# Kernel optimization log

Hardware: AMD Instinct MI355X
Metric: run time of the kernel (lower is better)

Reference implementation:

```python
import jax, jax.numpy as jnp
import numpy as np

NUM_NODES = 120000   # entity count
D = 128              # graph_emb_size
T = 10               # time_steps / train_year
B = 64               # batch of input_ids
R = 4                # num_rel
N = 64               # max neighbors per relation (padded)
C = 64               # TCN channel width (output_size)
I = 64               # influence_emb_size
K = 2                # kernel size
L = 8                # TCN levels (num_channels = [64]*8)


def _causal_conv(x, w, b, d):
    # x: [M, Cin, T], w: [Cout, Cin, k] -> causal dilated conv -> [M, Cout, T]
    pad = (w.shape[-1] - 1) * d
    y = jax.lax.conv_general_dilated(x, w, window_strides=(1,), padding=[(pad, 0)],
                                     rhs_dilation=(d,), dimension_numbers=('NCH', 'OIH', 'NCH'))
    return y + b[None, :, None]


def _tcn_last(x, w1_0, b1_0, w2_0, b2_0, down_w, down_b, w1, b1, w2, b2):
    # Bai-style TemporalConvNet; x: [M, D, T] -> last-step state [M, C]
    y = jax.nn.relu(_causal_conv(x, w1_0, b1_0, 1))
    y = jax.nn.relu(_causal_conv(y, w2_0, b2_0, 1))
    h = jax.nn.relu(y + _causal_conv(x, down_w, down_b, 1))  # 1x1 downsample residual (Cin != C)
    for i in range(1, L):
        d = 2 ** i
        y = jax.nn.relu(_causal_conv(h, w1[i - 1], b1[i - 1], d))
        y = jax.nn.relu(_causal_conv(y, w2[i - 1], b2[i - 1], d))
        h = jax.nn.relu(y + h)
    return h[..., -1]


def setup_inputs() -> dict:
    key = jax.random.key(0)
    ks = jax.random.split(key, 16)
    embeddings = jax.random.normal(ks[0], (T, NUM_NODES, D), jnp.float32)
    # entity -> per-year row index; negative = entity absent that year (zero-padded)
    alignment = jax.random.randint(ks[1], (NUM_NODES, T), -NUM_NODES // 5, NUM_NODES).astype(jnp.int32)
    neighbor_idx = jax.random.randint(ks[2], (B, R, N), 0, NUM_NODES).astype(jnp.int32)
    neighbor_mask = jax.random.randint(ks[3], (B, R, N), 0, 2).astype(bool)
    g = lambda k, sh, s: jax.random.normal(k, sh, jnp.float32) * s
    return {
        'embeddings': embeddings,
        'w1_0': g(ks[4], (R, C, D, K), (2.0 / (D * K)) ** 0.5),
        'b1_0': jnp.zeros((R, C), jnp.float32),
        'w2_0': g(ks[5], (R, C, C, K), (2.0 / (C * K)) ** 0.5),
        'b2_0': jnp.zeros((R, C), jnp.float32),
        'down_w': g(ks[6], (R, C, D, 1), (2.0 / D) ** 0.5),
        'down_b': jnp.zeros((R, C), jnp.float32),
        'w1': g(ks[7], (R, L - 1, C, C, K), (2.0 / (C * K)) ** 0.5),
        'b1': jnp.zeros((R, L - 1, C), jnp.float32),
        'w2': g(ks[8], (R, L - 1, C, C, K), (2.0 / (C * K)) ** 0.5),
        'b2': jnp.zeros((R, L - 1, C), jnp.float32),
        'rel_w': g(ks[9], (R, C, I), (2.0 / (C + I)) ** 0.5),
        'alignment': alignment,
        'neighbor_idx': neighbor_idx,
        'neighbor_mask': neighbor_mask,
    }


def reference(embeddings, w1_0, b1_0, w2_0, b2_0, down_w, down_b, w1, b1, w2, b2,
              rel_w, alignment, neighbor_idx, neighbor_mask):
    seq = alignment[neighbor_idx]                                   # [B,R,N,T]
    valid = (seq >= 0) & neighbor_mask[..., None]                   # per-year + existence mask
    idx = jnp.clip(seq, 0)
    # per-year gather: embeddings[t][idx[...,t]] -> [B,R,N,D,T]
    gath = jax.vmap(lambda e, i: e[i], in_axes=(0, -1), out_axes=-1)(embeddings, idx)
    x = gath * valid[:, :, :, None, :].astype(gath.dtype)           # zero-pad absent years
    x = jnp.transpose(x, (1, 0, 2, 3, 4)).reshape(R, B * N, D, T)   # relation-major, neighbors as batch
    last = jax.vmap(_tcn_last)(x, w1_0, b1_0, w2_0, b2_0, down_w, down_b, w1, b1, w2, b2)  # [R,B*N,C]
    infl = jnp.einsum('rmc,rci->rmi', last, rel_w).reshape(R, B, N, I)
    m = jnp.transpose(neighbor_mask, (1, 0, 2)).astype(infl.dtype)  # [R,B,N] drop padded neighbors
    return jnp.einsum('rbni,rbn->bi', infl, m)                      # sum over neighbors and relations
```

## Files before the change

kernel.cpp:

```cpp
#include <hip/hip_runtime.h>
#include <hip/hip_bf16.h>
#include <stdint.h>

constexpr int NUM_NODES = 120000;
constexpr int Tn = 10;
constexpr int Bb = 64, Rr = 4, Nn = 64, Cc = 64, Ii = 64;
constexpr int RSTR  = 147456;
constexpr int OFF0  = 0;
constexpr int OFF1  = 16384;
constexpr int OFF2  = 24576;
constexpr int OFFL0 = 32768;

constexpr int OFF_X  = 0;
constexpr int OFF_H0 = 0;
constexpr int OFF_H1 = 10240;
constexpr int OFF_H2 = 16384;
constexpr int OFF_H3 = 20480;
constexpr int OFF_Y  = 40960;
constexpr int ZOFF   = 61440;
constexpr int SMEMB  = 61696;

typedef __attribute__((ext_vector_type(8))) short bf16x8;
typedef __attribute__((ext_vector_type(4))) float f32x4;
typedef __attribute__((ext_vector_type(4))) short s16x4;

__device__ __forceinline__ short f2bf(float f) {
  __hip_bfloat16 h = __float2bfloat16(f);
  return *reinterpret_cast<short*>(&h);
}
__device__ __forceinline__ float bf2f(short s) {
  union { unsigned int u; float f; } x;
  x.u = ((unsigned int)(unsigned short)s) << 16;
  return x.f;
}

extern "C" __global__ void prep_kernel(const float* __restrict__ w1_0,
                                       const float* __restrict__ w2_0,
                                       const float* __restrict__ down_w,
                                       const float* __restrict__ w1s,
                                       const float* __restrict__ w2s,
                                       short* __restrict__ Wf) {
  int i0 = blockIdx.x * blockDim.x + threadIdx.x;
  int stride = gridDim.x * blockDim.x;
  for (int e = i0; e < Rr * RSTR; e += stride) {
    int r = e / RSTR, q = e - r * RSTR;
    float v;
    if (q < 16384) {
      int j = q & 7, lane = (q >> 3) & 63, ks = (q >> 9) & 3, ct = (q >> 11) & 3, tap = (q >> 13) & 1;
      int cout = ct * 16 + (lane & 15), cin = ks * 32 + (lane >> 4) * 8 + j;
      v = w1_0[((r * 64 + cout) * 128 + cin) * 2 + tap];
    } else if (q < 24576) {
      int q2 = q - 16384;
      int j = q2 & 7, lane = (q2 >> 3) & 63, ks = (q2 >> 9) & 3, ct = (q2 >> 11) & 3;
      int cout = ct * 16 + (lane & 15), cin = ks * 32 + (lane >> 4) * 8 + j;
      v = down_w[(r * 64 + cout) * 128 + cin];
    } else if (q < 32768) {
      int q2 = q - 24576;
      int j = q2 & 7, lane = (q2 >> 3) & 63, ks = (q2 >> 9) & 1, ct = (q2 >> 10) & 3, tap = (q2 >> 12) & 1;
      int cout = ct * 16 + (lane & 15), cin = ks * 32 + (lane >> 4) * 8 + j;
      v = w2_0[((r * 64 + cout) * 64 + cin) * 2 + tap];
    } else {
      int q2 = q - 32768;
      int lc = q2 >> 13;
      int l = lc >> 1, jw = lc & 1;
      int q3 = q2 & 8191;
      int j = q3 & 7, lane = (q3 >> 3) & 63, ks = (q3 >> 9) & 1, ct = (q3 >> 10) & 3, tap = (q3 >> 12) & 1;
      int cout = ct * 16 + (lane & 15), cin = ks * 32 + (lane >> 4) * 8 + j;
      const float* src = jw ? w2s : w1s;
      v = src[(((r * 7 + l) * 64 + cout) * 64 + cin) * 2 + tap];
    }
    Wf[e] = f2bf(v);
  }
}

template <int KSN, int NMT, int NTAP, int ROWB>
__device__ __forceinline__ void conv_sp(const char* __restrict__ sm, int srcOff,
                                        const short* __restrict__ wf1,
                                        const short* __restrict__ wf0,
                                        const float* __restrict__ bias,
                                        const int (&T1)[NMT], const int (&T0)[NMT],
                                        int lane, int ct, f32x4 (&acc)[NMT]) {
  const int c16 = (lane >> 4) * 16;
  const int sw = (lane & 7) << 4;
  const int cm = lane & 15;
  float bv[4];
#pragma unroll
  for (int g = 0; g < 4; ++g) bv[g] = bias[ct * 16 + (lane >> 4) * 4 + g];
#pragma unroll
  for (int mt = 0; mt < NMT; ++mt) acc[mt] = (f32x4){bv[0], bv[1], bv[2], bv[3]};
  bf16x8 af1[KSN], af0[KSN];
#pragma unroll
  for (int ks = 0; ks < KSN; ++ks)
    af1[ks] = *(const bf16x8*)(wf1 + ((ct * KSN + ks) * 64 + lane) * 8);
  if (NTAP == 2) {
#pragma unroll
    for (int ks = 0; ks < KSN; ++ks)
      af0[ks] = *(const bf16x8*)(wf0 + ((ct * KSN + ks) * 64 + lane) * 8);
  }
#pragma unroll
  for (int mt = 0; mt < NMT; ++mt) {
    int s1 = T1[mt];
    const char* p1 = sm + ((s1 < 0) ? ZOFF : srcOff + (s1 * 16 + cm) * ROWB);
#pragma unroll
    for (int ks = 0; ks < KSN; ++ks) {
      bf16x8 b = *(const bf16x8*)(p1 + ((ks * 64 + c16) ^ sw));
      acc[mt] = __builtin_amdgcn_mfma_f32_16x16x32_bf16(af1[ks], b, acc[mt], 0, 0, 0);
    }
    if (NTAP == 2) {
      int s0 = T0[mt];
      const char* p0 = sm + ((s0 < 0) ? ZOFF : srcOff + (s0 * 16 + cm) * ROWB);
#pragma unroll
      for (int ks = 0; ks < KSN; ++ks) {
        bf16x8 b = *(const bf16x8*)(p0 + ((ks * 64 + c16) ^ sw));
        acc[mt] = __builtin_amdgcn_mfma_f32_16x16x32_bf16(af0[ks], b, acc[mt], 0, 0, 0);
      }
    }
  }
}

template <int NMT>
__device__ __forceinline__ void store_sp(char* __restrict__ sm, int dstOff, int s0,
                                         int lane, int ct, const f32x4 (&v)[NMT]) {
  const int co = ct * 32 + (lane >> 4) * 8;
  const int sw = (lane & 7) << 4;
#pragma unroll
  for (int mt = 0; mt < NMT; ++mt) {
    int oc = (s0 + mt) * 16 + (lane & 15);
    s16x4 p;
#pragma unroll
    for (int g = 0; g < 4; ++g) p[g] = f2bf(v[mt][g]);
    *(s16x4*)(sm + dstOff + oc * 128 + (co ^ sw)) = p;
  }
}

#define RELU_ALL(A, N)                                        \
  _Pragma("unroll") for (int _t = 0; _t < N; ++_t)            \
      _Pragma("unroll") for (int _g = 0; _g < 4; ++_g)        \
          A[_t][_g] = fmaxf(A[_t][_g], 0.f);

template <int NMT>
__device__ __forceinline__ void resid_sp(const char* __restrict__ sm, int prevOff,
                                         const int (&R)[NMT], int lane, int ct,
                                         f32x4 (&a)[NMT]) {
  const int co = ct * 32 + (lane >> 4) * 8;
  const int sw = (lane & 7) << 4;
  const int cm = lane & 15;
#pragma unroll
  for (int mt = 0; mt < NMT; ++mt) {
    const char* p = sm + prevOff + (R[mt] * 16 + cm) * 128;
    s16x4 q = *(const s16x4*)(p + (co ^ sw));
#pragma unroll
    for (int g = 0; g < 4; ++g)
      a[mt][g] = fmaxf(fmaxf(a[mt][g], 0.f) + bf2f(q[g]), 0.f);
  }
}

extern "C" __global__ void __launch_bounds__(512, 4)
tcn_mfma(const float* __restrict__ emb, const int* __restrict__ align_,
         const int* __restrict__ nidx, const int* __restrict__ nmask,
         const float* __restrict__ b1_0, const float* __restrict__ b2_0,
         const float* __restrict__ down_b, const float* __restrict__ b1s,
         const float* __restrict__ b2s, const short* __restrict__ Wf,
         float* __restrict__ P) {
  __shared__ char sm[SMEMB];
  __shared__ int rowid[160];
  __shared__ float mkv[16];
  __shared__ int mapg[16];
  __shared__ int totv;

  const int tid = threadIdx.x;
  const int lane = tid & 63, wave = tid >> 6;
  const int ct = wave & 3, half = wave >> 2;
  const int blk = blockIdx.x;
  const int r = blk >> 8;
  const int b = (blk >> 2) & 63, chunk = blk & 3;

  if (tid < 64) {
    int n = tid;
    int msk = nmask[(b * Rr + r) * Nn + n];
    unsigned long long bal = __ballot(msk != 0);
    if (tid < 16) mapg[tid] = -1;
    if (tid == 0) totv = (int)__popcll(bal);
    int rank = (int)__popcll(bal & ((1ull << n) - 1ull));
    if (msk != 0 && rank >= chunk * 16 && rank < chunk * 16 + 16)
      mapg[rank - chunk * 16] = n;
  }
  if (tid >= 448 && tid < 480) *(uint64_t*)(sm + ZOFF + (tid - 448) * 8) = 0;
  __syncthreads();
  if (chunk * 16 >= totv) {
    if (tid < 64) P[((r * Bb + b) * 4 + chunk) * 64 + tid] = 0.f;
    return;
  }

  if (tid < 160) {
    int t = tid >> 4, seq = tid & 15;
    int n2 = mapg[seq];
    int s = -1;
    if (n2 >= 0) {
      int ent = nidx[(b * Rr + r) * Nn + n2];
      s = align_[ent * Tn + t];
    }
    rowid[tid] = (n2 >= 0 && s >= 0) ? s : -1;
    if (t == 0) mkv[seq] = (n2 >= 0) ? 1.0f : 0.0f;
  }
  __syncthreads();

#pragma unroll
  for (int it = 0; it < 10; ++it) {
    int idx = tid + it * 512;
    int col = idx >> 5, d4 = idx & 31;
    int row = rowid[col];
    int t = col >> 4;
    s16x4 p = {0, 0, 0, 0};
    if (row >= 0) {
      const float4 v = *(const float4*)(emb + ((size_t)t * NUM_NODES + row) * 128 + d4 * 4);
      p[0] = f2bf(v.x); p[1] = f2bf(v.y); p[2] = f2bf(v.z); p[3] = f2bf(v.w);
    }
    *(s16x4*)(sm + OFF_X + col * 256 + ((d4 * 8) ^ ((col & 7) << 4))) = p;
  }
  __syncthreads();

  const short* wr = Wf + r * RSTR;

  {
    static constexpr int T1a[5] = {0, 1, 2, 3, 4}, T0a[5] = {-1, 0, 1, 2, 3};
    static constexpr int T1b[5] = {5, 6, 7, 8, 9}, T0b[5] = {4, 5, 6, 7, 8};
    f32x4 a[5];
    conv_sp<4, 5, 2, 256>(sm, OFF_X, wr + OFF0 + 8192, wr + OFF0, b1_0 + r * 64,
                          half ? T1b : T1a, half ? T0b : T0a, lane, ct, a);
    RELU_ALL(a, 5)
    store_sp<5>(sm, OFF_Y, half ? 5 : 0, lane, ct, a);
  }
  f32x4 accD[3];
  {
    static constexpr int TDa[3] = {1, 3, 5}, TDb[3] = {5, 7, 9};
    conv_sp<4, 3, 1, 256>(sm, OFF_X, wr + OFF1, wr + OFF1, down_b + r * 64,
                          half ? TDb : TDa, half ? TDb : TDa, lane, ct, accD);
  }
  __syncthreads();
  {
    static constexpr int T1a[3] = {1, 3, 5}, T0a[3] = {0, 2, 4};
    static constexpr int T1b[3] = {5, 7, 9}, T0b[3] = {4, 6, 8};
    f32x4 a[3];
    conv_sp<2, 3, 2, 128>(sm, OFF_Y, wr + OFF2 + 4096, wr + OFF2, b2_0 + r * 64,
                          half ? T1b : T1a, half ? T0b : T0a, lane, ct, a);
#pragma unroll
    for (int mt = 0; mt < 3; ++mt)
#pragma unroll
      for (int g = 0; g < 4; ++g)
        a[mt][g] = fmaxf(fmaxf(a[mt][g], 0.f) + accD[mt][g], 0.f);
    store_sp<3>(sm, OFF_H0, half ? 2 : 0, lane, ct, a);
  }
  __syncthreads();
  {
    static constexpr int T1a[3] = {0, 1, 2}, T0a[3] = {-1, 0, 1};
    static constexpr int T1b[3] = {2, 3, 4}, T0b[3] = {1, 2, 3};
    const short* wl = wr + OFFL0;
    f32x4 a[3];
    conv_sp<2, 3, 2, 128>(sm, OFF_H0, wl + 4096, wl, b1s + (r * 7 + 0) * 64,
                          half ? T1b : T1a, half ? T0b : T0a, lane, ct, a);
    RELU_ALL(a, 3)
    store_sp<3>(sm, OFF_Y, half ? 2 : 0, lane, ct, a);
  }
  __syncthreads();
  {
    static constexpr int T1a[2] = {0, 2}, T0a[2] = {-1, 1}, Ra[2] = {0, 2};
    static constexpr int T1b[2] = {2, 4}, T0b[2] = {1, 3}, Rb[2] = {2, 4};
    const short* wl = wr + OFFL0 + 8192;
    f32x4 a[2];
    conv_sp<2, 2, 2, 128>(sm, OFF_Y, wl + 4096, wl, b2s + (r * 7 + 0) * 64,
                          half ? T1b : T1a, half ? T0b : T0a, lane, ct, a);
    resid_sp<2>(sm, OFF_H0, half ? Rb : Ra, lane, ct, a);
    store_sp<2>(sm, OFF_H1, half ? 1 : 0, lane, ct, a);
  }
  __syncthreads();
  {
    static constexpr int T1a[2] = {0, 1}, T0a[2] = {-1, 0};
    static constexpr int T1b[2] = {1, 2}, T0b[2] = {0, 1};
    const short* wl = wr + OFFL0 + 16384;
    f32x4 a[2];
    conv_sp<2, 2, 2, 128>(sm, OFF_H1, wl + 4096, wl, b1s + (r * 7 + 1) * 64,
                          half ? T1b : T1a, half ? T0b : T0a, lane, ct, a);
    RELU_ALL(a, 2)
    store_sp<2>(sm, OFF_Y, half ? 1 : 0, lane, ct, a);
  }
  __syncthreads();
  {
    static constexpr int T1a[1] = {0}, T0a[1] = {-1}, Ra[1] = {0};
    static constexpr int T1b[1] = {2}, T0b[1] = {1}, Rb[1] = {2};
    const short* wl = wr + OFFL0 + 16384 + 8192;
    f32x4 a[1];
    conv_sp<2, 1, 2, 128>(sm, OFF_Y, wl + 4096, wl, b2s + (r * 7 + 1) * 64,
                          half ? T1b : T1a, half ? T0b : T0a, lane, ct, a);
    resid_sp<1>(sm, OFF_H1, half ? Rb : Ra, lane, ct, a);
    store_sp<1>(sm, OFF_H2, half ? 1 : 0, lane, ct, a);
  }
  __syncthreads();
  {
    static constexpr int T1a[1] = {0}, T0a[1] = {-1};
    static constexpr int T1b[1] = {1}, T0b[1] = {0};
    const short* wl = wr + OFFL0 + 32768;
    f32x4 a[1];
    conv_sp<2, 1, 2, 128>(sm, OFF_H2, wl + 4096, wl, b1s + (r * 7 + 2) * 64,
                          half ? T1b : T1a, half ? T0b : T0a, lane, ct, a);
    RELU_ALL(a, 1)
    store_sp<1>(sm, OFF_Y, half ? 1 : 0, lane, ct, a);
  }
  __syncthreads();
  {
    static constexpr int T1c[1] = {1}, T0c[1] = {0}, Rc[1] = {1};
    const short* wl = wr + OFFL0 + 32768 + 8192;
    f32x4 a[1];
    conv_sp<2, 1, 2, 128>(sm, OFF_Y, wl + 4096, wl, b2s + (r * 7 + 2) * 64,
                          T1c, T0c, lane, ct, a);
    resid_sp<1>(sm, OFF_H2, Rc, lane, ct, a);
    store_sp<1>(sm, OFF_H3, 0, lane, ct, a);
  }
  __syncthreads();

  if (wave != 0) return;

  f32x4 hfin[4];
  static constexpr int TA[1] = {0};
#pragma unroll 1
  for (int li = 0; li < 4; ++li) {
    const short* base = wr + OFFL0 + (3 + li) * 16384;
    const int prevOff = OFF_H3 + li * 2048;
#pragma unroll
    for (int c2 = 0; c2 < 4; ++c2) {
      f32x4 a[1];
      conv_sp<2, 1, 1, 128>(sm, prevOff, base + 4096, base + 4096,
                            b1s + (r * 7 + 3 + li) * 64, TA, TA, lane, c2, a);
      RELU_ALL(a, 1)
      store_sp<1>(sm, OFF_Y, 0, lane, c2, a);
    }
    __builtin_amdgcn_s_waitcnt(0);
    __builtin_amdgcn_sched_barrier(0);
#pragma unroll
    for (int c2 = 0; c2 < 4; ++c2) {
      f32x4 a[1];
      conv_sp<2, 1, 1, 128>(sm, OFF_Y, base + 8192 + 4096, base + 8192 + 4096,
                            b2s + (r * 7 + 3 + li) * 64, TA, TA, lane, c2, a);
      resid_sp<1>(sm, prevOff, TA, lane, c2, a);
      if (li < 3) store_sp<1>(sm, prevOff + 2048, 0, lane, c2, a);
      hfin[c2] = a[0];
    }
    __builtin_amdgcn_s_waitcnt(0);
    __builtin_amdgcn_sched_barrier(0);
  }

  float mk = mkv[lane & 15];
#pragma unroll
  for (int c2 = 0; c2 < 4; ++c2) {
    float s0 = hfin[c2][0] * mk, s1 = hfin[c2][1] * mk;
    float s2 = hfin[c2][2] * mk, s3 = hfin[c2][3] * mk;
#pragma unroll
    for (int m2 = 1; m2 <= 8; m2 <<= 1) {
      s0 += __shfl_xor(s0, m2);
      s1 += __shfl_xor(s1, m2);
      s2 += __shfl_xor(s2, m2);
      s3 += __shfl_xor(s3, m2);
    }
    if ((lane & 15) == 0) {
      int base = ((r * Bb + b) * 4 + chunk) * 64 + c2 * 16 + (lane >> 4) * 4;
      P[base + 0] = s0;
      P[base + 1] = s1;
      P[base + 2] = s2;
      P[base + 3] = s3;
    }
  }
}

extern "C" __global__ void reduce_kernel(const float* __restrict__ P,
                                         const float* __restrict__ rel_w,
                                         float* __restrict__ out) {
  __shared__ float Sl[Rr * Cc];
  int b = blockIdx.x, i = threadIdx.x;
  for (int idx = i; idx < Rr * Cc; idx += 64) {
    int rr = idx >> 6, cc = idx & 63;
    float s = 0.f;
    for (int p = 0; p < 4; ++p) s += P[((rr * Bb + b) * 4 + p) * 64 + cc];
    Sl[idx] = s;
  }
  __syncthreads();
  float acc = 0.f;
  for (int r = 0; r < Rr; ++r)
#pragma unroll
    for (int cc = 0; cc < 64; ++cc)
      acc += Sl[r * Cc + cc] * rel_w[(r * Cc + cc) * Ii + i];
  out[b * Ii + i] = acc;
}

extern "C" void kernel_launch(void* const* d_in, const int* in_sizes, int n_in,
                              void* d_out, int out_size, void* d_ws, size_t ws_size,
                              hipStream_t stream) {
  const float* emb    = (const float*)d_in[0];
  const float* w1_0   = (const float*)d_in[1];
  const float* b1_0   = (const float*)d_in[2];
  const float* w2_0   = (const float*)d_in[3];
  const float* b2_0   = (const float*)d_in[4];
  const float* down_w = (const float*)d_in[5];
  const float* down_b = (const float*)d_in[6];
  const float* w1s    = (const float*)d_in[7];
  const float* b1s    = (const float*)d_in[8];
  const float* w2s    = (const float*)d_in[9];
  const float* b2s    = (const float*)d_in[10];
  const float* rel_w  = (const float*)d_in[11];
  const int* align_   = (const int*)d_in[12];
  const int* nidx     = (const int*)d_in[13];
  const int* nmask    = (const int*)d_in[14];

  float* P  = (float*)d_ws;
  short* Wf = (short*)((char*)d_ws + 524288);

  prep_kernel<<<768, 256, 0, stream>>>(w1_0, w2_0, down_w, w1s, w2s, Wf);
  tcn_mfma<<<1024, 512, 0, stream>>>(emb, align_, nidx, nmask, b1_0, b2_0, down_b,
                                     b1s, b2s, Wf, P);
  reduce_kernel<<<Bb, Cc, 0, stream>>>(P, rel_w, (float*)d_out);
}
```

Baseline: 63.00 us.

## Process 32 neighbors per block with 4 waves sharing weight fragments across two tiles

```diff
diff --git a/kernel.cpp b/kernel.cpp
--- a/kernel.cpp
+++ b/kernel.cpp
@@ -4,7 +4,7 @@
 
 constexpr int NUM_NODES = 120000;
 constexpr int Tn = 10;
-constexpr int Bb = 64, Rr = 4, Nn = 64, Cc = 64, Ii = 64;
+constexpr int Bb = 64, Rr = 4, Nn = 64, Ii = 64;
 constexpr int RSTR  = 147456;
 constexpr int OFF0  = 0;
 constexpr int OFF1  = 16384;
@@ -13,12 +13,13 @@
 
 constexpr int OFF_X  = 0;
 constexpr int OFF_H0 = 0;
-constexpr int OFF_H1 = 10240;
-constexpr int OFF_H2 = 16384;
-constexpr int OFF_H3 = 20480;
-constexpr int OFF_Y  = 40960;
-constexpr int ZOFF   = 61440;
-constexpr int SMEMB  = 61696;
+constexpr int OFF_H1 = 20480;
+constexpr int OFF_H2 = 32768;
+constexpr int OFF_H3 = 40960;
+constexpr int OFF_Y  = 81920;
+constexpr int ZOFF   = 122880;
+constexpr int POFF   = 123136;
+constexpr int SMEMB  = 123648;
 
 typedef __attribute__((ext_vector_type(8))) short bf16x8;
 typedef __attribute__((ext_vector_type(4))) float f32x4;
@@ -79,83 +80,90 @@
                                         const short* __restrict__ wf0,
                                         const float* __restrict__ bias,
                                         const int (&T1)[NMT], const int (&T0)[NMT],
-                                        int lane, int ct, f32x4 (&acc)[NMT]) {
-  const int c16 = (lane >> 4) * 16;
+                                        int lane, int c, int h, f32x4 (&acc)[NMT][2]) {
   const int sw = (lane & 7) << 4;
-  const int cm = lane & 15;
-  float bv[4];
-#pragma unroll
-  for (int g = 0; g < 4; ++g) bv[g] = bias[ct * 16 + (lane >> 4) * 4 + g];
-#pragma unroll
-  for (int mt = 0; mt < NMT; ++mt) acc[mt] = (f32x4){bv[0], bv[1], bv[2], bv[3]};
-  bf16x8 af1[KSN], af0[KSN];
-#pragma unroll
-  for (int ks = 0; ks < KSN; ++ks)
-    af1[ks] = *(const bf16x8*)(wf1 + ((ct * KSN + ks) * 64 + lane) * 8);
-  if (NTAP == 2) {
-#pragma unroll
-    for (int ks = 0; ks < KSN; ++ks)
-      af0[ks] = *(const bf16x8*)(wf0 + ((ct * KSN + ks) * 64 + lane) * 8);
-  }
-#pragma unroll
-  for (int mt = 0; mt < NMT; ++mt) {
-    int s1 = T1[mt];
-    const char* p1 = sm + ((s1 < 0) ? ZOFF : srcOff + (s1 * 16 + cm) * ROWB);
-#pragma unroll
-    for (int ks = 0; ks < KSN; ++ks) {
-      bf16x8 b = *(const bf16x8*)(p1 + ((ks * 64 + c16) ^ sw));
-      acc[mt] = __builtin_amdgcn_mfma_f32_16x16x32_bf16(af1[ks], b, acc[mt], 0, 0, 0);
-    }
+  const int colb = h * 16 + (lane & 15);
+  const int krow = (lane >> 4) * 16;
+  float bv[2][4];
+#pragma unroll
+  for (int i = 0; i < 2; ++i)
+#pragma unroll
+    for (int g = 0; g < 4; ++g) bv[i][g] = bias[(2 * c + i) * 16 + (lane >> 4) * 4 + g];
+#pragma unroll
+  for (int mt = 0; mt < NMT; ++mt)
+#pragma unroll
+    for (int i = 0; i < 2; ++i) acc[mt][i] = (f32x4){bv[i][0], bv[i][1], bv[i][2], bv[i][3]};
+#pragma unroll
+  for (int ks = 0; ks < KSN; ++ks) {
+    bf16x8 a1[2], a0[2];
+#pragma unroll
+    for (int i = 0; i < 2; ++i)
+      a1[i] = *(const bf16x8*)(wf1 + (((2 * c + i) * KSN + ks) * 64 + lane) * 8);
     if (NTAP == 2) {
-      int s0 = T0[mt];
-      const char* p0 = sm + ((s0 < 0) ? ZOFF : srcOff + (s0 * 16 + cm) * ROWB);
-#pragma unroll
-      for (int ks = 0; ks < KSN; ++ks) {
-        bf16x8 b = *(const bf16x8*)(p0 + ((ks * 64 + c16) ^ sw));
-        acc[mt] = __builtin_amdgcn_mfma_f32_16x16x32_bf16(af0[ks], b, acc[mt], 0, 0, 0);
+#pragma unroll
+      for (int i = 0; i < 2; ++i)
+        a0[i] = *(const bf16x8*)(wf0 + (((2 * c + i) * KSN + ks) * 64 + lane) * 8);
+    }
+#pragma unroll
+    for (int mt = 0; mt < NMT; ++mt) {
+      int s1 = T1[mt];
+      const char* p1 = sm + ((s1 < 0) ? ZOFF : srcOff + (s1 * 32 + colb) * ROWB);
+      bf16x8 b1 = *(const bf16x8*)(p1 + ((ks * 64 + krow) ^ sw));
+      acc[mt][0] = __builtin_amdgcn_mfma_f32_16x16x32_bf16(a1[0], b1, acc[mt][0], 0, 0, 0);
+      acc[mt][1] = __builtin_amdgcn_mfma_f32_16x16x32_bf16(a1[1], b1, acc[mt][1], 0, 0, 0);
+      if (NTAP == 2) {
+        int s0 = T0[mt];
+        const char* p0 = sm + ((s0 < 0) ? ZOFF : srcOff + (s0 * 32 + colb) * ROWB);
+        bf16x8 b0 = *(const bf16x8*)(p0 + ((ks * 64 + krow) ^ sw));
+        acc[mt][0] = __builtin_amdgcn_mfma_f32_16x16x32_bf16(a0[0], b0, acc[mt][0], 0, 0, 0);
+        acc[mt][1] = __builtin_amdgcn_mfma_f32_16x16x32_bf16(a0[1], b0, acc[mt][1], 0, 0, 0);
       }
     }
   }
 }
 
 template <int NMT>
-__device__ __forceinline__ void store_sp(char* __restrict__ sm, int dstOff, int s0,
-                                         int lane, int ct, const f32x4 (&v)[NMT]) {
-  const int co = ct * 32 + (lane >> 4) * 8;
+__device__ __forceinline__ void store_sp(char* __restrict__ sm, int dstOff, int lane,
+                                         int c, int h, const f32x4 (&v)[NMT][2]) {
   const int sw = (lane & 7) << 4;
-#pragma unroll
-  for (int mt = 0; mt < NMT; ++mt) {
-    int oc = (s0 + mt) * 16 + (lane & 15);
-    s16x4 p;
-#pragma unroll
-    for (int g = 0; g < 4; ++g) p[g] = f2bf(v[mt][g]);
-    *(s16x4*)(sm + dstOff + oc * 128 + (co ^ sw)) = p;
-  }
+  const int colb = h * 16 + (lane & 15);
+#pragma unroll
+  for (int mt = 0; mt < NMT; ++mt)
+#pragma unroll
+    for (int i = 0; i < 2; ++i) {
+      int co = (2 * c + i) * 32 + (lane >> 4) * 8;
+      s16x4 p;
+#pragma unroll
+      for (int g = 0; g < 4; ++g) p[g] = f2bf(v[mt][i][g]);
+      *(s16x4*)(sm + dstOff + (mt * 32 + colb) * 128 + (co ^ sw)) = p;
+    }
 }
 
 #define RELU_ALL(A, N)                                        \
   _Pragma("unroll") for (int _t = 0; _t < N; ++_t)            \
-      _Pragma("unroll") for (int _g = 0; _g < 4; ++_g)        \
-          A[_t][_g] = fmaxf(A[_t][_g], 0.f);
+      _Pragma("unroll") for (int _i = 0; _i < 2; ++_i)        \
+          _Pragma("unroll") for (int _g = 0; _g < 4; ++_g)    \
+              A[_t][_i][_g] = fmaxf(A[_t][_i][_g], 0.f);
 
 template <int NMT>
 __device__ __forceinline__ void resid_sp(const char* __restrict__ sm, int prevOff,
-                                         const int (&R)[NMT], int lane, int ct,
-                                         f32x4 (&a)[NMT]) {
-  const int co = ct * 32 + (lane >> 4) * 8;
+                                         const int (&R)[NMT], int lane, int c, int h,
+                                         f32x4 (&a)[NMT][2]) {
   const int sw = (lane & 7) << 4;
-  const int cm = lane & 15;
-#pragma unroll
-  for (int mt = 0; mt < NMT; ++mt) {
-    const char* p = sm + prevOff + (R[mt] * 16 + cm) * 128;
-    s16x4 q = *(const s16x4*)(p + (co ^ sw));
-#pragma unroll
-    for (int g = 0; g < 4; ++g)
-      a[mt][g] = fmaxf(fmaxf(a[mt][g], 0.f) + bf2f(q[g]), 0.f);
-  }
-}
-
-extern "C" __global__ void __launch_bounds__(512, 4)
+  const int colb = h * 16 + (lane & 15);
+#pragma unroll
+  for (int mt = 0; mt < NMT; ++mt)
+#pragma unroll
+    for (int i = 0; i < 2; ++i) {
+      int co = (2 * c + i) * 32 + (lane >> 4) * 8;
+      s16x4 q = *(const s16x4*)(sm + prevOff + (R[mt] * 32 + colb) * 128 + (co ^ sw));
+#pragma unroll
+      for (int g = 0; g < 4; ++g)
+        a[mt][i][g] = fmaxf(fmaxf(a[mt][i][g], 0.f) + bf2f(q[g]), 0.f);
+    }
+}
+
+extern "C" __global__ void __launch_bounds__(256, 1)
 tcn_mfma(const float* __restrict__ emb, const int* __restrict__ align_,
          const int* __restrict__ nidx, const int* __restrict__ nmask,
          const float* __restrict__ b1_0, const float* __restrict__ b2_0,
@@ -163,54 +171,54 @@
          const float* __restrict__ b2s, const short* __restrict__ Wf,
          float* __restrict__ P) {
   __shared__ char sm[SMEMB];
-  __shared__ int rowid[160];
-  __shared__ float mkv[16];
-  __shared__ int mapg[16];
+  __shared__ int rowid[320];
+  __shared__ float mkv[32];
+  __shared__ int mapg[32];
   __shared__ int totv;
 
   const int tid = threadIdx.x;
   const int lane = tid & 63, wave = tid >> 6;
-  const int ct = wave & 3, half = wave >> 2;
+  const int c = wave & 1, h = wave >> 1;
   const int blk = blockIdx.x;
-  const int r = blk >> 8;
-  const int b = (blk >> 2) & 63, chunk = blk & 3;
+  const int r = blk >> 7;
+  const int b = (blk >> 1) & 63, chunk = blk & 1;
 
   if (tid < 64) {
     int n = tid;
     int msk = nmask[(b * Rr + r) * Nn + n];
     unsigned long long bal = __ballot(msk != 0);
-    if (tid < 16) mapg[tid] = -1;
+    if (tid < 32) mapg[tid] = -1;
     if (tid == 0) totv = (int)__popcll(bal);
     int rank = (int)__popcll(bal & ((1ull << n) - 1ull));
-    if (msk != 0 && rank >= chunk * 16 && rank < chunk * 16 + 16)
-      mapg[rank - chunk * 16] = n;
-  }
-  if (tid >= 448 && tid < 480) *(uint64_t*)(sm + ZOFF + (tid - 448) * 8) = 0;
-  __syncthreads();
-  if (chunk * 16 >= totv) {
-    if (tid < 64) P[((r * Bb + b) * 4 + chunk) * 64 + tid] = 0.f;
+    if (msk != 0 && rank >= chunk * 32 && rank < chunk * 32 + 32)
+      mapg[rank - chunk * 32] = n;
+  }
+  if (tid >= 192 && tid < 224) *(uint64_t*)(sm + ZOFF + (tid - 192) * 8) = 0;
+  __syncthreads();
+  if (chunk * 32 >= totv) {
+    if (tid < 64) P[((r * Bb + b) * 2 + chunk) * 64 + tid] = 0.f;
     return;
   }
 
-  if (tid < 160) {
-    int t = tid >> 4, seq = tid & 15;
+  for (int i2 = tid; i2 < 320; i2 += 256) {
+    int t = i2 >> 5, seq = i2 & 31;
     int n2 = mapg[seq];
     int s = -1;
     if (n2 >= 0) {
       int ent = nidx[(b * Rr + r) * Nn + n2];
       s = align_[ent * Tn + t];
     }
-    rowid[tid] = (n2 >= 0 && s >= 0) ? s : -1;
+    rowid[i2] = (n2 >= 0 && s >= 0) ? s : -1;
     if (t == 0) mkv[seq] = (n2 >= 0) ? 1.0f : 0.0f;
   }
   __syncthreads();
 
 #pragma unroll
-  for (int it = 0; it < 10; ++it) {
-    int idx = tid + it * 512;
+  for (int it = 0; it < 40; ++it) {
+    int idx = tid + it * 256;
     int col = idx >> 5, d4 = idx & 31;
     int row = rowid[col];
-    int t = col >> 4;
+    int t = col >> 5;
     s16x4 p = {0, 0, 0, 0};
     if (row >= 0) {
       const float4 v = *(const float4*)(emb + ((size_t)t * NUM_NODES + row) * 128 + d4 * 4);
@@ -223,137 +231,129 @@
   const short* wr = Wf + r * RSTR;
 
   {
-    static constexpr int T1a[5] = {0, 1, 2, 3, 4}, T0a[5] = {-1, 0, 1, 2, 3};
-    static constexpr int T1b[5] = {5, 6, 7, 8, 9}, T0b[5] = {4, 5, 6, 7, 8};
-    f32x4 a[5];
-    conv_sp<4, 5, 2, 256>(sm, OFF_X, wr + OFF0 + 8192, wr + OFF0, b1_0 + r * 64,
-                          half ? T1b : T1a, half ? T0b : T0a, lane, ct, a);
+    static constexpr int T1[10] = {0, 1, 2, 3, 4, 5, 6, 7, 8, 9};
+    static constexpr int T0[10] = {-1, 0, 1, 2, 3, 4, 5, 6, 7, 8};
+    f32x4 a[10][2];
+    conv_sp<4, 10, 2, 256>(sm, OFF_X, wr + OFF0 + 8192, wr + OFF0, b1_0 + r * 64,
+                           T1, T0, lane, c, h, a);
+    RELU_ALL(a, 10)
+    store_sp<10>(sm, OFF_Y, lane, c, h, a);
+  }
+  f32x4 accD[5][2];
+  {
+    static constexpr int TD[5] = {1, 3, 5, 7, 9};
+    conv_sp<4, 5, 1, 256>(sm, OFF_X, wr + OFF1, wr + OFF1, down_b + r * 64,
+                          TD, TD, lane, c, h, accD);
+  }
+  __syncthreads();
+  {
+    static constexpr int T1[5] = {1, 3, 5, 7, 9}, T0[5] = {0, 2, 4, 6, 8};
+    f32x4 a[5][2];
+    conv_sp<2, 5, 2, 128>(sm, OFF_Y, wr + OFF2 + 4096, wr + OFF2, b2_0 + r * 64,
+                          T1, T0, lane, c, h, a);
+#pragma unroll
+    for (int mt = 0; mt < 5; ++mt)
+#pragma unroll
+      for (int i = 0; i < 2; ++i)
+#pragma unroll
+        for (int g = 0; g < 4; ++g)
+          a[mt][i][g] = fmaxf(fmaxf(a[mt][i][g], 0.f) + accD[mt][i][g], 0.f);
+    store_sp<5>(sm, OFF_H0, lane, c, h, a);
+  }
+  __syncthreads();
+  {
+    static constexpr int T1[5] = {0, 1, 2, 3, 4}, T0[5] = {-1, 0, 1, 2, 3};
+    const short* wl = wr + OFFL0;
+    f32x4 a[5][2];
+    conv_sp<2, 5, 2, 128>(sm, OFF_H0, wl + 4096, wl, b1s + (r * 7 + 0) * 64,
+                          T1, T0, lane, c, h, a);
     RELU_ALL(a, 5)
-    store_sp<5>(sm, OFF_Y, half ? 5 : 0, lane, ct, a);
-  }
-  f32x4 accD[3];
-  {
-    static constexpr int TDa[3] = {1, 3, 5}, TDb[3] = {5, 7, 9};
-    conv_sp<4, 3, 1, 256>(sm, OFF_X, wr + OFF1, wr + OFF1, down_b + r * 64,
-                          half ? TDb : TDa, half ? TDb : TDa, lane, ct, accD);
-  }
-  __syncthreads();
-  {
-    static constexpr int T1a[3] = {1, 3, 5}, T0a[3] = {0, 2, 4};
-    static constexpr int T1b[3] = {5, 7, 9}, T0b[3] = {4, 6, 8};
-    f32x4 a[3];
-    conv_sp<2, 3, 2, 128>(sm, OFF_Y, wr + OFF2 + 4096, wr + OFF2, b2_0 + r * 64,
-                          half ? T1b : T1a, half ? T0b : T0a, lane, ct, a);
-#pragma unroll
-    for (int mt = 0; mt < 3; ++mt)
-#pragma unroll
-      for (int g = 0; g < 4; ++g)
-        a[mt][g] = fmaxf(fmaxf(a[mt][g], 0.f) + accD[mt][g], 0.f);
-    store_sp<3>(sm, OFF_H0, half ? 2 : 0, lane, ct, a);
-  }
-  __syncthreads();
-  {
-    static constexpr int T1a[3] = {0, 1, 2}, T0a[3] = {-1, 0, 1};
-    static constexpr int T1b[3] = {2, 3, 4}, T0b[3] = {1, 2, 3};
-    const short* wl = wr + OFFL0;
-    f32x4 a[3];
-    conv_sp<2, 3, 2, 128>(sm, OFF_H0, wl + 4096, wl, b1s + (r * 7 + 0) * 64,
-                          half ? T1b : T1a, half ? T0b : T0a, lane, ct, a);
+    store_sp<5>(sm, OFF_Y, lane, c, h, a);
+  }
+  __syncthreads();
+  {
+    static constexpr int T1[3] = {0, 2, 4}, T0[3] = {-1, 1, 3}, R[3] = {0, 2, 4};
+    const short* wl = wr + OFFL0 + 8192;
+    f32x4 a[3][2];
+    conv_sp<2, 3, 2, 128>(sm, OFF_Y, wl + 4096, wl, b2s + (r * 7 + 0) * 64,
+                          T1, T0, lane, c, h, a);
+    resid_sp<3>(sm, OFF_H0, R, lane, c, h, a);
+    store_sp<3>(sm, OFF_H1, lane, c, h, a);
+  }
+  __syncthreads();
+  {
+    static constexpr int T1[3] = {0, 1, 2}, T0[3] = {-1, 0, 1};
+    const short* wl = wr + OFFL0 + 16384;
+    f32x4 a[3][2];
+    conv_sp<2, 3, 2, 128>(sm, OFF_H1, wl + 4096, wl, b1s + (r * 7 + 1) * 64,
+                          T1, T0, lane, c, h, a);
     RELU_ALL(a, 3)
-    store_sp<3>(sm, OFF_Y, half ? 2 : 0, lane, ct, a);
-  }
-  __syncthreads();
-  {
-    static constexpr int T1a[2] = {0, 2}, T0a[2] = {-1, 1}, Ra[2] = {0, 2};
-    static constexpr int T1b[2] = {2, 4}, T0b[2] = {1, 3}, Rb[2] = {2, 4};
-    const short* wl = wr + OFFL0 + 8192;
-    f32x4 a[2];
-    conv_sp<2, 2, 2, 128>(sm, OFF_Y, wl + 4096, wl, b2s + (r * 7 + 0) * 64,
-                          half ? T1b : T1a, half ? T0b : T0a, lane, ct, a);
-    resid_sp<2>(sm, OFF_H0, half ? Rb : Ra, lane, ct, a);
-    store_sp<2>(sm, OFF_H1, half ? 1 : 0, lane, ct, a);
-  }
-  __syncthreads();
-  {
-    static constexpr int T1a[2] = {0, 1}, T0a[2] = {-1, 0};
-    static constexpr int T1b[2] = {1, 2}, T0b[2] = {0, 1};
-    const short* wl = wr + OFFL0 + 16384;
-    f32x4 a[2];
-    conv_sp<2, 2, 2, 128>(sm, OFF_H1, wl + 4096, wl, b1s + (r * 7 + 1) * 64,
-                          half ? T1b : T1a, half ? T0b : T0a, lane, ct, a);
+    store_sp<3>(sm, OFF_Y, lane, c, h, a);
+  }
+  __syncthreads();
+  {
+    static constexpr int T1[2] = {0, 2}, T0[2] = {-1, 1}, R[2] = {0, 2};
+    const short* wl = wr + OFFL0 + 16384 + 8192;
+    f32x4 a[2][2];
+    conv_sp<2, 2, 2, 128>(sm, OFF_Y, wl + 4096, wl, b2s + (r * 7 + 1) * 64,
+                          T1, T0, lane, c, h, a);
+    resid_sp<2>(sm, OFF_H1, R, lane, c, h, a);
+    store_sp<2>(sm, OFF_H2, lane, c, h, a);
+  }
+  __syncthreads();
+  {
+    static constexpr int T1[2] = {0, 1}, T0[2] = {-1, 0};
+    const short* wl = wr + OFFL0 + 32768;
+    f32x4 a[2][2];
+    conv_sp<2, 2, 2, 128>(sm, OFF_H2, wl + 4096, wl, b1s + (r * 7 + 2) * 64,
+                          T1, T0, lane, c, h, a);
     RELU_ALL(a, 2)
-    store_sp<2>(sm, OFF_Y, half ? 1 : 0, lane, ct, a);
-  }
-  __syncthreads();
-  {
-    static constexpr int T1a[1] = {0}, T0a[1] = {-1}, Ra[1] = {0};
-    static constexpr int T1b[1] = {2}, T0b[1] = {1}, Rb[1] = {2};
-    const short* wl = wr + OFFL0 + 16384 + 8192;
-    f32x4 a[1];
-    conv_sp<2, 1, 2, 128>(sm, OFF_Y, wl + 4096, wl, b2s + (r * 7 + 1) * 64,
-                          half ? T1b : T1a, half ? T0b : T0a, lane, ct, a);
-    resid_sp<1>(sm, OFF_H1, half ? Rb : Ra, lane, ct, a);
-    store_sp<1>(sm, OFF_H2, half ? 1 : 0, lane, ct, a);
-  }
-  __syncthreads();
-  {
-    static constexpr int T1a[1] = {0}, T0a[1] = {-1};
-    static constexpr int T1b[1] = {1}, T0b[1] = {0};
-    const short* wl = wr + OFFL0 + 32768;
-    f32x4 a[1];
-    conv_sp<2, 1, 2, 128>(sm, OFF_H2, wl + 4096, wl, b1s + (r * 7 + 2) * 64,
-                          half ? T1b : T1a, half ? T0b : T0a, lane, ct, a);
-    RELU_ALL(a, 1)
-    store_sp<1>(sm, OFF_Y, half ? 1 : 0, lane, ct, a);
-  }
-  __syncthreads();
-  {
-    static constexpr int T1c[1] = {1}, T0c[1] = {0}, Rc[1] = {1};
+    store_sp<2>(sm, OFF_Y, lane, c, h, a);
+  }
+  __syncthreads();
+  {
+    static constexpr int T1[1] = {1}, T0[1] = {0}, R[1] = {1};
     const short* wl = wr + OFFL0 + 32768 + 8192;
-    f32x4 a[1];
+    f32x4 a[1][2];
     conv_sp<2, 1, 2, 128>(sm, OFF_Y, wl + 4096, wl, b2s + (r * 7 + 2) * 64,
-                          T1c, T0c, lane, ct, a);
-    resid_sp<1>(sm, OFF_H2, Rc, lane, ct, a);
-    store_sp<1>(sm, OFF_H3, 0, lane, ct, a);
-  }
-  __syncthreads();
-
-  if (wave != 0) return;
-
-  f32x4 hfin[4];
+                          T1, T0, lane, c, h, a);
+    resid_sp<1>(sm, OFF_H2, R, lane, c, h, a);
+    store_sp<1>(sm, OFF_H3, lane, c, h, a);
+  }
+  __syncthreads();
+
+  f32x4 hfin[1][2];
   static constexpr int TA[1] = {0};
 #pragma unroll 1
   for (int li = 0; li < 4; ++li) {
     const short* base = wr + OFFL0 + (3 + li) * 16384;
-    const int prevOff = OFF_H3 + li * 2048;
-#pragma unroll
-    for (int c2 = 0; c2 < 4; ++c2) {
-      f32x4 a[1];
+    const int prevOff = OFF_H3 + li * 4096;
+    {
+      f32x4 a[1][2];
       conv_sp<2, 1, 1, 128>(sm, prevOff, base + 4096, base + 4096,
-                            b1s + (r * 7 + 3 + li) * 64, TA, TA, lane, c2, a);
+                            b1s + (r * 7 + 3 + li) * 64, TA, TA, lane, c, h, a);
       RELU_ALL(a, 1)
-      store_sp<1>(sm, OFF_Y, 0, lane, c2, a);
-    }
-    __builtin_amdgcn_s_waitcnt(0);
-    __builtin_amdgcn_sched_barrier(0);
-#pragma unroll
-    for (int c2 = 0; c2 < 4; ++c2) {
-      f32x4 a[1];
+      store_sp<1>(sm, OFF_Y, lane, c, h, a);
+    }
+    __syncthreads();
+    {
+      f32x4 a[1][2];
       conv_sp<2, 1, 1, 128>(sm, OFF_Y, base + 8192 + 4096, base + 8192 + 4096,
-                            b2s + (r * 7 + 3 + li) * 64, TA, TA, lane, c2, a);
-      resid_sp<1>(sm, prevOff, TA, lane, c2, a);
-      if (li < 3) store_sp<1>(sm, prevOff + 2048, 0, lane, c2, a);
-      hfin[c2] = a[0];
-    }
-    __builtin_amdgcn_s_waitcnt(0);
-    __builtin_amdgcn_sched_barrier(0);
-  }
-
-  float mk = mkv[lane & 15];
-#pragma unroll
-  for (int c2 = 0; c2 < 4; ++c2) {
-    float s0 = hfin[c2][0] * mk, s1 = hfin[c2][1] * mk;
-    float s2 = hfin[c2][2] * mk, s3 = hfin[c2][3] * mk;
+                            b2s + (r * 7 + 3 + li) * 64, TA, TA, lane, c, h, a);
+      resid_sp<1>(sm, prevOff, TA, lane, c, h, a);
+      if (li < 3) store_sp<1>(sm, prevOff + 4096, lane, c, h, a);
+      hfin[0][0] = a[0][0];
+      hfin[0][1] = a[0][1];
+    }
+    __syncthreads();
+  }
+
+  float mk = mkv[h * 16 + (lane & 15)];
+  float* part = (float*)(sm + POFF);
+#pragma unroll
+  for (int i = 0; i < 2; ++i) {
+    float s0 = hfin[0][i][0] * mk, s1 = hfin[0][i][1] * mk;
+    float s2 = hfin[0][i][2] * mk, s3 = hfin[0][i][3] * mk;
 #pragma unroll
     for (int m2 = 1; m2 <= 8; m2 <<= 1) {
       s0 += __shfl_xor(s0, m2);
@@ -362,32 +362,38 @@
       s3 += __shfl_xor(s3, m2);
     }
     if ((lane & 15) == 0) {
-      int base = ((r * Bb + b) * 4 + chunk) * 64 + c2 * 16 + (lane >> 4) * 4;
-      P[base + 0] = s0;
-      P[base + 1] = s1;
-      P[base + 2] = s2;
-      P[base + 3] = s3;
-    }
+      int cl = i * 16 + (lane >> 4) * 4;
+      part[(c * 2 + h) * 32 + cl + 0] = s0;
+      part[(c * 2 + h) * 32 + cl + 1] = s1;
+      part[(c * 2 + h) * 32 + cl + 2] = s2;
+      part[(c * 2 + h) * 32 + cl + 3] = s3;
+    }
+  }
+  __syncthreads();
+  if (tid < 64) {
+    int c2 = tid >> 5, cl = tid & 31;
+    float val = part[(c2 * 2 + 0) * 32 + cl] + part[(c2 * 2 + 1) * 32 + cl];
+    P[((r * Bb + b) * 2 + chunk) * 64 + tid] = val;
   }
 }
 
 extern "C" __global__ void reduce_kernel(const float* __restrict__ P,
                                          const float* __restrict__ rel_w,
                                          float* __restrict__ out) {
-  __shared__ float Sl[Rr * Cc];
+  __shared__ float Sl[Rr * 64];
   int b = blockIdx.x, i = threadIdx.x;
-  for (int idx = i; idx < Rr * Cc; idx += 64) {
+  for (int idx = i; idx < Rr * 64; idx += 64) {
     int rr = idx >> 6, cc = idx & 63;
     float s = 0.f;
-    for (int p = 0; p < 4; ++p) s += P[((rr * Bb + b) * 4 + p) * 64 + cc];
+    for (int p = 0; p < 2; ++p) s += P[((rr * Bb + b) * 2 + p) * 64 + cc];
     Sl[idx] = s;
   }
   __syncthreads();
   float acc = 0.f;
-  for (int r = 0; r < Rr; ++r)
+  for (int rr = 0; rr < Rr; ++rr)
 #pragma unroll
     for (int cc = 0; cc < 64; ++cc)
-      acc += Sl[r * Cc + cc] * rel_w[(r * Cc + cc) * Ii + i];
+      acc += Sl[rr * 64 + cc] * rel_w[(rr * 64 + cc) * Ii + i];
   out[b * Ii + i] = acc;
 }
 
@@ -414,7 +420,7 @@
   short* Wf = (short*)((char*)d_ws + 524288);
 
   prep_kernel<<<768, 256, 0, stream>>>(w1_0, w2_0, down_w, w1s, w2s, Wf);
-  tcn_mfma<<<1024, 512, 0, stream>>>(emb, align_, nidx, nmask, b1_0, b2_0, down_b,
-                                     b1s, b2s, Wf, P);
-  reduce_kernel<<<Bb, Cc, 0, stream>>>(P, rel_w, (float*)d_out);
-}
+  tcn_mfma<<<512, 256, 0, stream>>>(emb, align_, nidx, nmask, b1_0, b2_0, down_b,
+                                    b1s, b2s, Wf, P);
+  reduce_kernel<<<Bb, 64, 0, stream>>>(P, rel_w, (float*)d_out);
+}
```

New measurement: 76.65 us. 1.22x slower.
